# Optimization experiments

Measured on AMD Instinct MI355X. Metric: run time of the kernel, lower is better.

Reference implementation:

```python
import jax, jax.numpy as jnp
import numpy as np

SEMA_DIM = 1024
L1, L2, B = 256, 320, 64


def setup_inputs() -> dict:
    key = jax.random.key(0)
    k1, k2, kw1, kb1, kw2, kb2 = jax.random.split(key, 6)
    D = SEMA_DIM
    s = 1.0 / np.sqrt(D)
    return {
        "r1": jax.random.normal(k1, (L1, B, D), dtype=jnp.float32),
        "r2": jax.random.normal(k2, (L2, B, D), dtype=jnp.float32),
        "W1": jax.random.uniform(kw1, (D, D), jnp.float32, -s, s),
        "b1": jax.random.uniform(kb1, (D,), jnp.float32, -s, s),
        "W2": jax.random.uniform(kw2, (D, D), jnp.float32, -s, s),
        "b2": jax.random.uniform(kb2, (D,), jnp.float32, -s, s),
    }


def _mlp(x, W1, b1, W2, b2):
    # torch Linear: x @ W.T + b
    h = jax.nn.relu(x @ W1.T + b1)
    return h @ W2.T + b2


def reference(r1, r2, W1, b1, W2, b2):
    # (L, B, D) -> mlp -> (B, L, D)
    r1 = jnp.transpose(_mlp(r1, W1, b1, W2, b2), (1, 0, 2))  # [B, L1, D]
    r2 = jnp.transpose(_mlp(r2, W1, b1, W2, b2), (1, 0, 2))  # [B, L2, D]

    o = jnp.einsum("bid,bjd->bij", r1, r2)  # [B, L1, L2]
    o1 = jax.nn.softmax(o, axis=2)           # attend r1 -> r2
    o2 = jax.nn.softmax(o, axis=1)           # attend r2 -> r1

    r1_c = jnp.einsum("bij,bjd->bid", o1, r2)  # [B, L1, D]
    r2_c = jnp.einsum("bij,bid->bjd", o2, r1)  # [B, L2, D]

    r1_pool = jnp.concatenate([r1, r1_c], axis=-1).sum(axis=1) / r1.shape[1]  # [B, 2D]
    r2_pool = jnp.concatenate([r2, r2_c], axis=-1).sum(axis=1) / r2.shape[1]  # [B, 2D]
    return (r1_pool, r2_pool)
```

## Files before the change

kernel.cpp:

```cpp
#include <hip/hip_runtime.h>
#include <stdint.h>

#define L1C 256
#define L2C 320
#define BC  64
#define DC  1024

typedef __bf16 bf16_t;
typedef __bf16 bf16x8 __attribute__((ext_vector_type(8)));
typedef __bf16 bf16x4 __attribute__((ext_vector_type(4)));
typedef float  f32x4  __attribute__((ext_vector_type(4)));

__device__ __forceinline__ void gload16(const void* g, void* l) {
  __builtin_amdgcn_global_load_lds(
      (__attribute__((address_space(1))) void*)g,
      (__attribute__((address_space(3))) void*)l, 16, 0, 0);
}

__global__ __launch_bounds__(256)
void conv_kernel(const float* __restrict__ src, bf16_t* __restrict__ dst, int n4) {
  int i = blockIdx.x * 256 + threadIdx.x;
  const int stride = gridDim.x * 256;
  for (; i < n4; i += stride) {
    float4 v = ((const float4*)src)[i];
    bf16x4 o = { (__bf16)v.x, (__bf16)v.y, (__bf16)v.z, (__bf16)v.w };
    ((bf16x4*)dst)[i] = o;
  }
}

__global__ __launch_bounds__(512, 2)
void mlp_gemm8(const bf16_t* __restrict__ A, const bf16_t* __restrict__ W,
               const float* __restrict__ bias, bf16_t* __restrict__ C,
               int Mtiles, int relu) {
  const int nwg = Mtiles * 4;
  const int cpx = nwg >> 3;
  const int wg  = ((int)blockIdx.x & 7) * cpx + ((int)blockIdx.x >> 3);
  const int mt = wg >> 2, nt = wg & 3;

  __shared__ __align__(16) char lds[131072];

  const int t    = threadIdx.x;
  const int lane = t & 63, wid = t >> 6;
  const int wm = wid >> 2, wn = wid & 3;
  const int rsel = lane & 15, hi = lane >> 4;
  const int t16 = t * 16;

  const int P0 = t16, P1 = 8192 + t16;
  const int Lg0 = P0 ^ ((P0 >> 3) & 0x30);
  const int Lg1 = P1 ^ ((P1 >> 3) & 0x30);
  const int rS0 = Lg0 >> 6, cS0 = (Lg0 & 63) >> 1;
  const int rS1 = Lg1 >> 6, cS1 = (Lg1 & 63) >> 1;
  const bf16_t* pA0 = A + (size_t)(mt * 256 + rS0) * 1024 + cS0;
  const bf16_t* pA1 = A + (size_t)(mt * 256 + rS1) * 1024 + cS1;
  const bf16_t* pB0 = W + (size_t)(nt * 256 + rS0) * 1024 + cS0;
  const bf16_t* pB1 = W + (size_t)(nt * 256 + rS1) * 1024 + cS1;

  const int kchunk = (hi ^ ((rsel >> 1) & 3)) << 4;
  const int offA = ((wm * 128 + rsel) << 6) + kchunk;
  const int offB = 16384 + ((wn * 64 + rsel) << 6) + kchunk;

  f32x4 acc[8][4] = {};
  bf16x8 bfr[4];

#pragma unroll
  for (int p = 0; p < 3; ++p) {
    char* db = lds + p * 32768;
    gload16(pA0 + p * 32, db + t16);
    gload16(pA1 + p * 32, db + 8192 + t16);
    gload16(pB0 + p * 32, db + 16384 + t16);
    gload16(pB1 + p * 32, db + 24576 + t16);
  }
  asm volatile("s_waitcnt vmcnt(8)" ::: "memory");
  __builtin_amdgcn_s_barrier();
  __builtin_amdgcn_sched_barrier(0);

#pragma unroll 1
  for (int tt = 0; tt < 32; ++tt) {
    const char* rb = lds + (tt & 3) * 32768;
    char* sb = lds + ((tt + 3) & 3) * 32768;
    const int ks = (tt + 3) * 32;
    bf16x8 af[4];
#pragma unroll
    for (int m = 0; m < 4; ++m) af[m] = *(const bf16x8*)(rb + offA + m * 1024);
#pragma unroll
    for (int n = 0; n < 4; ++n) bfr[n] = *(const bf16x8*)(rb + offB + n * 1024);
    if (tt < 29) {
      gload16(pA0 + ks, sb + t16);
      gload16(pA1 + ks, sb + 8192 + t16);
    }
    __builtin_amdgcn_s_setprio(1);
#pragma unroll
    for (int m = 0; m < 4; ++m)
#pragma unroll
      for (int n = 0; n < 4; ++n)
        acc[m][n] = __builtin_amdgcn_mfma_f32_16x16x32_bf16(af[m], bfr[n], acc[m][n], 0, 0, 0);
    __builtin_amdgcn_s_setprio(0);
    __builtin_amdgcn_s_barrier();
    __builtin_amdgcn_sched_barrier(0);
#pragma unroll
    for (int m = 0; m < 4; ++m) af[m] = *(const bf16x8*)(rb + offA + (m + 4) * 1024);
    if (tt < 29) {
      gload16(pB0 + ks, sb + 16384 + t16);
      gload16(pB1 + ks, sb + 24576 + t16);
    }
    __builtin_amdgcn_s_setprio(1);
#pragma unroll
    for (int m = 0; m < 4; ++m)
#pragma unroll
      for (int n = 0; n < 4; ++n)
        acc[m + 4][n] = __builtin_amdgcn_mfma_f32_16x16x32_bf16(af[m], bfr[n], acc[m + 4][n], 0, 0, 0);
    __builtin_amdgcn_s_setprio(0);
    if (tt < 29)       asm volatile("s_waitcnt vmcnt(8)" ::: "memory");
    else if (tt == 29) asm volatile("s_waitcnt vmcnt(4)" ::: "memory");
    else if (tt == 30) asm volatile("s_waitcnt vmcnt(0)" ::: "memory");
    __builtin_amdgcn_s_barrier();
    __builtin_amdgcn_sched_barrier(0);
  }

  const int row0 = mt * 256 + wm * 128 + hi * 4;
  const int col0 = nt * 256 + wn * 64 + rsel;
  float bv[4];
#pragma unroll
  for (int n = 0; n < 4; ++n) bv[n] = bias[col0 + n * 16];
#pragma unroll
  for (int m = 0; m < 8; ++m) {
#pragma unroll
    for (int q = 0; q < 4; ++q) {
      const size_t rr = (size_t)(row0 + m * 16 + q) * 1024;
#pragma unroll
      for (int n = 0; n < 4; ++n) {
        float v = acc[m][n][q] + bv[n];
        if (relu) v = fmaxf(v, 0.f);
        C[rr + col0 + n * 16] = (bf16_t)v;
      }
    }
  }
}

__global__ __launch_bounds__(256)
void logits_gemm(const bf16_t* __restrict__ Y, float* __restrict__ O) {
  const int wg = ((int)blockIdx.x & 7) * 48 + ((int)blockIdx.x >> 3);
  const int b = wg / 6, t = wg % 6;
  const int mt = t / 3, nt = t % 3;

  const int f = threadIdx.x;
  const int lane = f & 63, w = f >> 6;
  const int sRow = f >> 2, sCol8 = (f & 3) * 8;

  const bf16_t* Y1 = Y;
  const bf16_t* Y2 = Y + (size_t)L1C * BC * DC;

  const int i0 = mt * 128 + sRow;
  const int i1 = i0 + 64;
  int j0 = nt * 128 + sRow;      if (j0 > L2C - 1) j0 = L2C - 1;
  int j1 = nt * 128 + sRow + 64; if (j1 > L2C - 1) j1 = L2C - 1;
  const bf16_t* A0 = Y1 + ((size_t)i0 * BC + b) * DC + sCol8;
  const bf16_t* A1 = Y1 + ((size_t)i1 * BC + b) * DC + sCol8;
  const bf16_t* B0 = Y2 + ((size_t)j0 * BC + b) * DC + sCol8;
  const bf16_t* B1 = Y2 + ((size_t)j1 * BC + b) * DC + sCol8;

  __shared__ __align__(16) bf16_t sA[128 * 32];
  __shared__ __align__(16) bf16_t sB[128 * 32];
  bf16_t* sAp = sA + sRow * 32 + sCol8;
  bf16_t* sBp = sB + sRow * 32 + sCol8;

  const int wr = (w >> 1) * 64, wc = (w & 1) * 64;
  const int rsel = lane & 15, koff = (lane >> 4) * 8;
  const bf16_t* rA = sA + (wr + rsel) * 32 + koff;
  const bf16_t* rB = sB + (wc + rsel) * 32 + koff;

  f32x4 acc[4][4] = {};
  for (int kt = 0; kt < 1024; kt += 32) {
    __syncthreads();
    gload16(A0 + kt, sAp);
    gload16(A1 + kt, sAp + 64 * 32);
    gload16(B0 + kt, sBp);
    gload16(B1 + kt, sBp + 64 * 32);
    asm volatile("s_waitcnt vmcnt(0)" ::: "memory");
    __syncthreads();
    bf16x8 af[4], bfv[4];
#pragma unroll
    for (int m = 0; m < 4; ++m) af[m] = *(const bf16x8*)(rA + m * 16 * 32);
#pragma unroll
    for (int n = 0; n < 4; ++n) bfv[n] = *(const bf16x8*)(rB + n * 16 * 32);
#pragma unroll
    for (int m = 0; m < 4; ++m)
#pragma unroll
      for (int n = 0; n < 4; ++n)
        acc[m][n] = __builtin_amdgcn_mfma_f32_16x16x32_bf16(af[m], bfv[n], acc[m][n], 0, 0, 0);
  }

  float* Ob = O + (size_t)b * L1C * L2C;
  const int row0 = mt * 128 + wr + (lane >> 4) * 4;
  const int col0 = nt * 128 + wc + rsel;
#pragma unroll
  for (int n = 0; n < 4; ++n) {
    const int c = col0 + n * 16;
    if (c < L2C) {
#pragma unroll
      for (int m = 0; m < 4; ++m) {
        const int r = row0 + m * 16;
#pragma unroll
        for (int q = 0; q < 4; ++q)
          Ob[(size_t)(r + q) * L2C + c] = acc[m][n][q];
      }
    }
  }
}

__global__ __launch_bounds__(256)
void row_stats(const float* __restrict__ O, float* __restrict__ rowM,
               float* __restrict__ rowInv) {
  const int gw = blockIdx.x * 4 + (threadIdx.x >> 6);
  const int lane = threadIdx.x & 63;
  const float* row = O + (size_t)gw * L2C;
  float v[5];
  float m = -1e30f;
#pragma unroll
  for (int t = 0; t < 5; ++t) { v[t] = row[t * 64 + lane]; m = fmaxf(m, v[t]); }
#pragma unroll
  for (int off = 32; off; off >>= 1) m = fmaxf(m, __shfl_xor(m, off));
  float s = 0.f;
#pragma unroll
  for (int t = 0; t < 5; ++t) s += __expf(v[t] - m);
#pragma unroll
  for (int off = 32; off; off >>= 1) s += __shfl_xor(s, off);
  if (lane == 0) { rowM[gw] = m; rowInv[gw] = 1.f / s; }
}

__global__ __launch_bounds__(256)
void col_stats_c1(const float* __restrict__ O, const float* __restrict__ rowM,
                  const float* __restrict__ rowInv, float* __restrict__ colM,
                  float* __restrict__ colInv, float* __restrict__ c1) {
  const int b = blockIdx.x / 5, jb = blockIdx.x % 5;
  const int jl = threadIdx.x & 63, ig = threadIdx.x >> 6;
  const int j = jb * 64 + jl;
  const float* Ob = O + (size_t)b * L1C * L2C + j;
  const float* rM = rowM + b * L1C;
  const float* rI = rowInv + b * L1C;
  float m = -1e30f, s = 0.f, cp = 0.f;
  for (int i = ig; i < L1C; i += 4) {
    float v = Ob[(size_t)i * L2C];
    float mn = fmaxf(m, v);
    s = s * __expf(m - mn) + __expf(v - mn);
    m = mn;
    cp += __expf(v - rM[i]) * rI[i];
  }
  __shared__ float sm[4][64], ss[4][64], sc[4][64];
  sm[ig][jl] = m; ss[ig][jl] = s; sc[ig][jl] = cp;
  __syncthreads();
  if (ig == 0) {
    for (int g = 1; g < 4; ++g) {
      float mg = sm[g][jl], sg = ss[g][jl];
      float mn = fmaxf(m, mg);
      s = s * __expf(m - mn) + sg * __expf(mg - mn);
      m = mn;
      cp += sc[g][jl];
    }
    colM[b * L2C + j] = m;
    colInv[b * L2C + j] = 1.f / s;
    c1[b * L2C + j] = cp;
  }
}

__global__ __launch_bounds__(256)
void c2_kernel(const float* __restrict__ O, const float* __restrict__ colM,
               const float* __restrict__ colInv, float* __restrict__ c2) {
  const int gw = blockIdx.x * 4 + (threadIdx.x >> 6);
  const int lane = threadIdx.x & 63;
  const int b = gw >> 8;
  const float* row = O + (size_t)gw * L2C;
  const float* cM = colM + b * L2C;
  const float* cI = colInv + b * L2C;
  float s = 0.f;
#pragma unroll
  for (int t = 0; t < 5; ++t) {
    const int j = t * 64 + lane;
    s += __expf(row[j] - cM[j]) * cI[j];
  }
#pragma unroll
  for (int off = 32; off; off >>= 1) s += __shfl_xor(s, off);
  if (lane == 0) c2[gw] = s;
}

__global__ __launch_bounds__(256)
void pool_y1(const bf16_t* __restrict__ Y1, const float* __restrict__ c2,
             float* __restrict__ out) {
  const int b = blockIdx.x >> 2;
  const int d = (blockIdx.x & 3) * 256 + threadIdx.x;
  float s1 = 0.f, s2 = 0.f;
  const float* c2b = c2 + b * L1C;
  for (int i = 0; i < L1C; ++i) {
    float v = (float)Y1[((size_t)i * BC + b) * DC + d];
    s1 += v;
    s2 += c2b[i] * v;
  }
  out[(size_t)b * 2048 + d] = s1 * (1.f / L1C);
  out[(size_t)BC * 2048 + (size_t)b * 2048 + 1024 + d] = s2 * (1.f / L2C);
}

__global__ __launch_bounds__(256)
void pool_y2(const bf16_t* __restrict__ Y2, const float* __restrict__ c1,
             float* __restrict__ out) {
  const int b = blockIdx.x >> 2;
  const int d = (blockIdx.x & 3) * 256 + threadIdx.x;
  float s1 = 0.f, s2 = 0.f;
  const float* c1b = c1 + b * L2C;
  for (int j = 0; j < L2C; ++j) {
    float v = (float)Y2[((size_t)j * BC + b) * DC + d];
    s1 += v;
    s2 += c1b[j] * v;
  }
  out[(size_t)BC * 2048 + (size_t)b * 2048 + d] = s1 * (1.f / L2C);
  out[(size_t)b * 2048 + 1024 + d] = s2 * (1.f / L1C);
}

extern "C" void kernel_launch(void* const* d_in, const int* in_sizes, int n_in,
                              void* d_out, int out_size, void* d_ws, size_t ws_size,
                              hipStream_t stream) {
  const float* r1 = (const float*)d_in[0];
  const float* r2 = (const float*)d_in[1];
  const float* W1 = (const float*)d_in[2];
  const float* b1 = (const float*)d_in[3];
  const float* W2 = (const float*)d_in[4];
  const float* b2 = (const float*)d_in[5];
  float* out = (float*)d_out;
  char* ws = (char*)d_ws;

  const size_t M1 = (size_t)L1C * BC;
  const size_t M2 = (size_t)L2C * BC;
  const size_t Mt = M1 + M2;

  size_t off = 0;
  bf16_t* XB  = (bf16_t*)(ws + off); off += Mt * DC * 2;
  bf16_t* HB  = (bf16_t*)(ws + off); off += Mt * DC * 2;
  bf16_t* WB1 = (bf16_t*)(ws + off); off += (size_t)DC * DC * 2;
  bf16_t* WB2 = (bf16_t*)(ws + off); off += (size_t)DC * DC * 2;
  float* rowM   = (float*)(ws + off); off += 65536;
  float* rowInv = (float*)(ws + off); off += 65536;
  float* colM   = (float*)(ws + off); off += 81920;
  float* colInv = (float*)(ws + off); off += 81920;
  float* c1v    = (float*)(ws + off); off += 81920;
  float* c2v    = (float*)(ws + off); off += 65536;

  bf16_t* YB = XB;
  float*  O  = (float*)HB;

  conv_kernel<<<2048, 256, 0, stream>>>(r1, XB,            (int)(M1 * DC / 4));
  conv_kernel<<<2048, 256, 0, stream>>>(r2, XB + M1 * DC,  (int)(M2 * DC / 4));
  conv_kernel<<<512,  256, 0, stream>>>(W1, WB1, (int)((size_t)DC * DC / 4));
  conv_kernel<<<512,  256, 0, stream>>>(W2, WB2, (int)((size_t)DC * DC / 4));

  mlp_gemm8<<<576, 512, 0, stream>>>(XB, WB1, b1, HB, 144, 1);
  mlp_gemm8<<<576, 512, 0, stream>>>(HB, WB2, b2, YB, 144, 0);

  logits_gemm<<<384, 256, 0, stream>>>(YB, O);

  row_stats<<<4096, 256, 0, stream>>>(O, rowM, rowInv);
  col_stats_c1<<<320, 256, 0, stream>>>(O, rowM, rowInv, colM, colInv, c1v);
  c2_kernel<<<4096, 256, 0, stream>>>(O, colM, colInv, c2v);

  pool_y1<<<256, 256, 0, stream>>>(YB, c2v, out);
  pool_y2<<<256, 256, 0, stream>>>(YB + M1 * DC, c1v, out);
}
```

Before: 331.2 us.

## Refactor logits and pooling algebraically through W2 to skip second MLP GEMM

Expresses the logits as H1·(W2ᵀW2)·H2ᵀ plus per-row and per-column bias terms (H·W2ᵀb2), so the full second MLP layer over all L1+L2 rows is no longer computed. The pooled outputs are built by pooling H first and applying W2 to only 256 pooled rows in a small GEMM. The cost is extra precomputation: a W2 transpose, a Gram-matrix GEMM, a bias-projection vector, and bias terms threaded through the softmax stats kernels. It also adds bf16 rounding of the Gram matrix and of the pooled vectors, and the pool GEMM runs on only 16 workgroups.

```diff
diff --git a/kernel.cpp b/kernel.cpp
--- a/kernel.cpp
+++ b/kernel.cpp
@@ -25,6 +25,39 @@
     float4 v = ((const float4*)src)[i];
     bf16x4 o = { (__bf16)v.x, (__bf16)v.y, (__bf16)v.z, (__bf16)v.w };
     ((bf16x4*)dst)[i] = o;
+  }
+}
+
+__global__ __launch_bounds__(256)
+void w2t_kernel(const float* __restrict__ W2, bf16_t* __restrict__ W2T) {
+  __shared__ float tile[32][33];
+  const int tx = threadIdx.x & 31, ty = threadIdx.x >> 5;
+  const int x0 = blockIdx.x * 32, y0 = blockIdx.y * 32;
+#pragma unroll
+  for (int k = 0; k < 32; k += 8)
+    tile[ty + k][tx] = W2[(size_t)(y0 + ty + k) * 1024 + x0 + tx];
+  __syncthreads();
+#pragma unroll
+  for (int k = 0; k < 32; k += 8)
+    W2T[(size_t)(x0 + ty + k) * 1024 + y0 + tx] = (bf16_t)tile[tx][ty + k];
+}
+
+__global__ __launch_bounds__(256)
+void wb_kernel(const float* __restrict__ W2, const float* __restrict__ b2,
+               float* __restrict__ w2b) {
+  const int dt = threadIdx.x & 15, kg = threadIdx.x >> 4;
+  const int d = blockIdx.x * 16 + dt;
+  float s = 0.f;
+  for (int k = kg * 64; k < kg * 64 + 64; ++k)
+    s += W2[(size_t)k * 1024 + d] * b2[k];
+  __shared__ float red[16][17];
+  red[kg][dt] = s;
+  __syncthreads();
+  if (kg == 0) {
+    float t = 0.f;
+#pragma unroll
+    for (int g = 0; g < 16; ++g) t += red[g][dt];
+    w2b[d] = t;
   }
 }
 
@@ -138,7 +171,160 @@
 }
 
 __global__ __launch_bounds__(256)
-void logits_gemm(const bf16_t* __restrict__ Y, float* __restrict__ O) {
+void mlp_gemm(const bf16_t* __restrict__ A, const bf16_t* __restrict__ W,
+              const float* __restrict__ bias, bf16_t* __restrict__ C,
+              int Mtiles, int relu) {
+  const int nwg = Mtiles * 8;
+  const int wg  = ((int)blockIdx.x & 7) * (nwg >> 3) + ((int)blockIdx.x >> 3);
+  const int mt = wg >> 3, nt = wg & 7;
+
+  const int f = threadIdx.x;
+  const int lane = f & 63, w = f >> 6;
+  const int sRow = f >> 2, sCol8 = (f & 3) * 8;
+
+  const bf16_t* Ab = A + (size_t)mt * 128 * 1024 + (size_t)sRow * 1024 + sCol8;
+  const bf16_t* Bb = W + (size_t)nt * 128 * 1024 + (size_t)sRow * 1024 + sCol8;
+
+  __shared__ __align__(16) bf16_t sA[128 * 32];
+  __shared__ __align__(16) bf16_t sB[128 * 32];
+  bf16_t* sAp = sA + sRow * 32 + sCol8;
+  bf16_t* sBp = sB + sRow * 32 + sCol8;
+
+  const int wr = (w >> 1) * 64, wc = (w & 1) * 64;
+  const int rsel = lane & 15, koff = (lane >> 4) * 8;
+  const bf16_t* rA = sA + (wr + rsel) * 32 + koff;
+  const bf16_t* rB = sB + (wc + rsel) * 32 + koff;
+
+  f32x4 acc[4][4] = {};
+  for (int kt = 0; kt < 1024; kt += 32) {
+    __syncthreads();
+    gload16(Ab + kt,             sAp);
+    gload16(Ab + kt + 64 * 1024, sAp + 64 * 32);
+    gload16(Bb + kt,             sBp);
+    gload16(Bb + kt + 64 * 1024, sBp + 64 * 32);
+    asm volatile("s_waitcnt vmcnt(0)" ::: "memory");
+    __syncthreads();
+    bf16x8 af[4], bfv[4];
+#pragma unroll
+    for (int m = 0; m < 4; ++m) af[m] = *(const bf16x8*)(rA + m * 16 * 32);
+#pragma unroll
+    for (int n = 0; n < 4; ++n) bfv[n] = *(const bf16x8*)(rB + n * 16 * 32);
+#pragma unroll
+    for (int m = 0; m < 4; ++m)
+#pragma unroll
+      for (int n = 0; n < 4; ++n)
+        acc[m][n] = __builtin_amdgcn_mfma_f32_16x16x32_bf16(af[m], bfv[n], acc[m][n], 0, 0, 0);
+  }
+
+  const int row0 = mt * 128 + wr + (lane >> 4) * 4;
+  const int col0 = nt * 128 + wc + rsel;
+#pragma unroll
+  for (int n = 0; n < 4; ++n) {
+    const int c = col0 + n * 16;
+    const float bv = bias[c];
+#pragma unroll
+    for (int m = 0; m < 4; ++m) {
+      const int r = row0 + m * 16;
+#pragma unroll
+      for (int q = 0; q < 4; ++q) {
+        float v = acc[m][n][q] + bv;
+        if (relu) v = fmaxf(v, 0.f);
+        C[(size_t)(r + q) * 1024 + c] = (bf16_t)v;
+      }
+    }
+  }
+}
+
+__global__ __launch_bounds__(256)
+void pool_gemm(const bf16_t* __restrict__ A, const bf16_t* __restrict__ W,
+               const float* __restrict__ bias, float* __restrict__ out) {
+  const int nwg = 16;
+  const int wg  = ((int)blockIdx.x & 7) * (nwg >> 3) + ((int)blockIdx.x >> 3);
+  const int mt = wg >> 3, nt = wg & 7;
+
+  const int f = threadIdx.x;
+  const int lane = f & 63, w = f >> 6;
+  const int sRow = f >> 2, sCol8 = (f & 3) * 8;
+
+  const bf16_t* Ab = A + (size_t)mt * 128 * 1024 + (size_t)sRow * 1024 + sCol8;
+  const bf16_t* Bb = W + (size_t)nt * 128 * 1024 + (size_t)sRow * 1024 + sCol8;
+
+  __shared__ __align__(16) bf16_t sA[128 * 32];
+  __shared__ __align__(16) bf16_t sB[128 * 32];
+  bf16_t* sAp = sA + sRow * 32 + sCol8;
+  bf16_t* sBp = sB + sRow * 32 + sCol8;
+
+  const int wr = (w >> 1) * 64, wc = (w & 1) * 64;
+  const int rsel = lane & 15, koff = (lane >> 4) * 8;
+  const bf16_t* rA = sA + (wr + rsel) * 32 + koff;
+  const bf16_t* rB = sB + (wc + rsel) * 32 + koff;
+
+  f32x4 acc[4][4] = {};
+  for (int kt = 0; kt < 1024; kt += 32) {
+    __syncthreads();
+    gload16(Ab + kt,             sAp);
+    gload16(Ab + kt + 64 * 1024, sAp + 64 * 32);
+    gload16(Bb + kt,             sBp);
+    gload16(Bb + kt + 64 * 1024, sBp + 64 * 32);
+    asm volatile("s_waitcnt vmcnt(0)" ::: "memory");
+    __syncthreads();
+    bf16x8 af[4], bfv[4];
+#pragma unroll
+    for (int m = 0; m < 4; ++m) af[m] = *(const bf16x8*)(rA + m * 16 * 32);
+#pragma unroll
+    for (int n = 0; n < 4; ++n) bfv[n] = *(const bf16x8*)(rB + n * 16 * 32);
+#pragma unroll
+    for (int m = 0; m < 4; ++m)
+#pragma unroll
+      for (int n = 0; n < 4; ++n)
+        acc[m][n] = __builtin_amdgcn_mfma_f32_16x16x32_bf16(af[m], bfv[n], acc[m][n], 0, 0, 0);
+  }
+
+  const int row0 = mt * 128 + wr + (lane >> 4) * 4;
+  const int col0 = nt * 128 + wc + rsel;
+#pragma unroll
+  for (int n = 0; n < 4; ++n) {
+    const int c = col0 + n * 16;
+    const float bv = bias[c];
+#pragma unroll
+    for (int m = 0; m < 4; ++m) {
+      const int r = row0 + m * 16;
+#pragma unroll
+      for (int q = 0; q < 4; ++q) {
+        const int rg = r + q;
+        const size_t oo = (size_t)(rg >> 7) * 131072 + (size_t)(rg & 63) * 2048 +
+                          ((rg >> 6) & 1) * 1024 + c;
+        out[oo] = acc[m][n][q] + bv;
+      }
+    }
+  }
+}
+
+__global__ __launch_bounds__(256)
+void t_kernel(const bf16_t* __restrict__ H, const float* __restrict__ w2b,
+              float* __restrict__ tT1, float* __restrict__ tT2) {
+  const int wv = threadIdx.x >> 6, lane = threadIdx.x & 63;
+  const int r = blockIdx.x * 4 + wv;
+  const bf16_t* hrow = H + (size_t)r * 1024;
+  float s = 0.f;
+#pragma unroll
+  for (int h = 0; h < 2; ++h) {
+    bf16x8 v = *(const bf16x8*)(hrow + h * 512 + lane * 8);
+#pragma unroll
+    for (int e = 0; e < 8; ++e) s += (float)v[e] * w2b[h * 512 + lane * 8 + e];
+  }
+#pragma unroll
+  for (int off = 32; off; off >>= 1) s += __shfl_xor(s, off);
+  if (lane == 0) {
+    const int b = r & 63;
+    if (r < 16384) tT1[b * L1C + (r >> 6)] = s;
+    else           tT2[b * L2C + ((r - 16384) >> 6)] = s;
+  }
+}
+
+__global__ __launch_bounds__(256)
+void logits_gemm(const bf16_t* __restrict__ Y1, const bf16_t* __restrict__ Y2,
+                 float* __restrict__ O) {
   const int wg = ((int)blockIdx.x & 7) * 48 + ((int)blockIdx.x >> 3);
   const int b = wg / 6, t = wg % 6;
   const int mt = t / 3, nt = t % 3;
@@ -146,9 +332,6 @@
   const int f = threadIdx.x;
   const int lane = f & 63, w = f >> 6;
   const int sRow = f >> 2, sCol8 = (f & 3) * 8;
-
-  const bf16_t* Y1 = Y;
-  const bf16_t* Y2 = Y + (size_t)L1C * BC * DC;
 
   const int i0 = mt * 128 + sRow;
   const int i1 = i0 + 64;
@@ -209,15 +392,17 @@
 }
 
 __global__ __launch_bounds__(256)
-void row_stats(const float* __restrict__ O, float* __restrict__ rowM,
-               float* __restrict__ rowInv) {
+void row_stats(const float* __restrict__ O, const float* __restrict__ tT2,
+               float* __restrict__ rowM, float* __restrict__ rowInv) {
   const int gw = blockIdx.x * 4 + (threadIdx.x >> 6);
   const int lane = threadIdx.x & 63;
+  const int b = gw >> 8;
   const float* row = O + (size_t)gw * L2C;
+  const float* t2 = tT2 + b * L2C;
   float v[5];
   float m = -1e30f;
 #pragma unroll
-  for (int t = 0; t < 5; ++t) { v[t] = row[t * 64 + lane]; m = fmaxf(m, v[t]); }
+  for (int t = 0; t < 5; ++t) { v[t] = row[t * 64 + lane] + t2[t * 64 + lane]; m = fmaxf(m, v[t]); }
 #pragma unroll
   for (int off = 32; off; off >>= 1) m = fmaxf(m, __shfl_xor(m, off));
   float s = 0.f;
@@ -229,22 +414,27 @@
 }
 
 __global__ __launch_bounds__(256)
-void col_stats_c1(const float* __restrict__ O, const float* __restrict__ rowM,
-                  const float* __restrict__ rowInv, float* __restrict__ colM,
-                  float* __restrict__ colInv, float* __restrict__ c1) {
+void col_stats_c1(const float* __restrict__ O, const float* __restrict__ tT1,
+                  const float* __restrict__ tT2,
+                  const float* __restrict__ rowM, const float* __restrict__ rowInv,
+                  float* __restrict__ colM, float* __restrict__ colInv,
+                  float* __restrict__ c1) {
   const int b = blockIdx.x / 5, jb = blockIdx.x % 5;
   const int jl = threadIdx.x & 63, ig = threadIdx.x >> 6;
   const int j = jb * 64 + jl;
   const float* Ob = O + (size_t)b * L1C * L2C + j;
   const float* rM = rowM + b * L1C;
   const float* rI = rowInv + b * L1C;
+  const float* t1 = tT1 + b * L1C;
+  const float t2j = tT2[b * L2C + j];
   float m = -1e30f, s = 0.f, cp = 0.f;
   for (int i = ig; i < L1C; i += 4) {
-    float v = Ob[(size_t)i * L2C];
+    float ov = Ob[(size_t)i * L2C];
+    float v = ov + t1[i];
     float mn = fmaxf(m, v);
     s = s * __expf(m - mn) + __expf(v - mn);
     m = mn;
-    cp += __expf(v - rM[i]) * rI[i];
+    cp += __expf(ov + t2j - rM[i]) * rI[i];
   }
   __shared__ float sm[4][64], ss[4][64], sc[4][64];
   sm[ig][jl] = m; ss[ig][jl] = s; sc[ig][jl] = cp;
@@ -264,19 +454,21 @@
 }
 
 __global__ __launch_bounds__(256)
-void c2_kernel(const float* __restrict__ O, const float* __restrict__ colM,
-               const float* __restrict__ colInv, float* __restrict__ c2) {
+void c2_kernel(const float* __restrict__ O, const float* __restrict__ tT1,
+               const float* __restrict__ colM, const float* __restrict__ colInv,
+               float* __restrict__ c2) {
   const int gw = blockIdx.x * 4 + (threadIdx.x >> 6);
   const int lane = threadIdx.x & 63;
   const int b = gw >> 8;
   const float* row = O + (size_t)gw * L2C;
   const float* cM = colM + b * L2C;
   const float* cI = colInv + b * L2C;
+  const float t1i = tT1[b * L1C + (gw & 255)];
   float s = 0.f;
 #pragma unroll
   for (int t = 0; t < 5; ++t) {
     const int j = t * 64 + lane;
-    s += __expf(row[j] - cM[j]) * cI[j];
+    s += __expf(row[j] + t1i - cM[j]) * cI[j];
   }
 #pragma unroll
   for (int off = 32; off; off >>= 1) s += __shfl_xor(s, off);
@@ -284,35 +476,26 @@
 }
 
 __global__ __launch_bounds__(256)
-void pool_y1(const bf16_t* __restrict__ Y1, const float* __restrict__ c2,
-             float* __restrict__ out) {
+void u_kernel(const bf16_t* __restrict__ H, const float* __restrict__ c1,
+              const float* __restrict__ c2, bf16_t* __restrict__ Ub) {
   const int b = blockIdx.x >> 2;
   const int d = (blockIdx.x & 3) * 256 + threadIdx.x;
-  float s1 = 0.f, s2 = 0.f;
+  const bf16_t* H2 = H + (size_t)L1C * BC * DC;
+  float s1 = 0.f, s1c = 0.f, s2 = 0.f, s2c = 0.f;
   const float* c2b = c2 + b * L1C;
   for (int i = 0; i < L1C; ++i) {
-    float v = (float)Y1[((size_t)i * BC + b) * DC + d];
-    s1 += v;
-    s2 += c2b[i] * v;
-  }
-  out[(size_t)b * 2048 + d] = s1 * (1.f / L1C);
-  out[(size_t)BC * 2048 + (size_t)b * 2048 + 1024 + d] = s2 * (1.f / L2C);
-}
-
-__global__ __launch_bounds__(256)
-void pool_y2(const bf16_t* __restrict__ Y2, const float* __restrict__ c1,
-             float* __restrict__ out) {
-  const int b = blockIdx.x >> 2;
-  const int d = (blockIdx.x & 3) * 256 + threadIdx.x;
-  float s1 = 0.f, s2 = 0.f;
+    float v = (float)H[((size_t)i * BC + b) * DC + d];
+    s1 += v; s1c += c2b[i] * v;
+  }
   const float* c1b = c1 + b * L2C;
   for (int j = 0; j < L2C; ++j) {
-    float v = (float)Y2[((size_t)j * BC + b) * DC + d];
-    s1 += v;
-    s2 += c1b[j] * v;
-  }
-  out[(size_t)BC * 2048 + (size_t)b * 2048 + d] = s1 * (1.f / L2C);
-  out[(size_t)b * 2048 + 1024 + d] = s2 * (1.f / L1C);
+    float v = (float)H2[((size_t)j * BC + b) * DC + d];
+    s2 += v; s2c += c1b[j] * v;
+  }
+  Ub[(size_t)(0 * 64 + b) * 1024 + d] = (bf16_t)(s1  * (1.f / L1C));
+  Ub[(size_t)(1 * 64 + b) * 1024 + d] = (bf16_t)(s2c * (1.f / L1C));
+  Ub[(size_t)(2 * 64 + b) * 1024 + d] = (bf16_t)(s2  * (1.f / L2C));
+  Ub[(size_t)(3 * 64 + b) * 1024 + d] = (bf16_t)(s1c * (1.f / L2C));
 }
 
 extern "C" void kernel_launch(void* const* d_in, const int* in_sizes, int n_in,
@@ -336,30 +519,45 @@
   bf16_t* HB  = (bf16_t*)(ws + off); off += Mt * DC * 2;
   bf16_t* WB1 = (bf16_t*)(ws + off); off += (size_t)DC * DC * 2;
   bf16_t* WB2 = (bf16_t*)(ws + off); off += (size_t)DC * DC * 2;
-  float* rowM   = (float*)(ws + off); off += 65536;
-  float* rowInv = (float*)(ws + off); off += 65536;
-  float* colM   = (float*)(ws + off); off += 81920;
-  float* colInv = (float*)(ws + off); off += 81920;
-  float* c1v    = (float*)(ws + off); off += 81920;
-  float* c2v    = (float*)(ws + off); off += 65536;
-
-  bf16_t* YB = XB;
-  float*  O  = (float*)HB;
-
-  conv_kernel<<<2048, 256, 0, stream>>>(r1, XB,            (int)(M1 * DC / 4));
-  conv_kernel<<<2048, 256, 0, stream>>>(r2, XB + M1 * DC,  (int)(M2 * DC / 4));
+  bf16_t* W2T = (bf16_t*)(ws + off); off += (size_t)DC * DC * 2;
+  bf16_t* GB  = (bf16_t*)(ws + off); off += (size_t)DC * DC * 2;
+  float* w2b   = (float*)(ws + off); off += 4096;
+  float* zb    = (float*)(ws + off); off += 4096;
+  float* tT1   = (float*)(ws + off); off += BC * L1C * 4;
+  float* tT2   = (float*)(ws + off); off += BC * L2C * 4;
+  float* rowM  = (float*)(ws + off); off += BC * L1C * 4;
+  float* rowIv = (float*)(ws + off); off += BC * L1C * 4;
+  float* colM  = (float*)(ws + off); off += BC * L2C * 4;
+  float* colIv = (float*)(ws + off); off += BC * L2C * 4;
+  float* c1v   = (float*)(ws + off); off += BC * L2C * 4;
+  float* c2v   = (float*)(ws + off); off += BC * L1C * 4;
+  bf16_t* Ub   = (bf16_t*)(ws + off); off += 256 * DC * 2;
+
+  bf16_t* Z = XB;
+  float*  O = (float*)((char*)XB + 35651584);
+  bf16_t* H2 = HB + M1 * DC;
+
+  conv_kernel<<<2048, 256, 0, stream>>>(r1, XB,           (int)(M1 * DC / 4));
+  conv_kernel<<<2048, 256, 0, stream>>>(r2, XB + M1 * DC, (int)(M2 * DC / 4));
   conv_kernel<<<512,  256, 0, stream>>>(W1, WB1, (int)((size_t)DC * DC / 4));
   conv_kernel<<<512,  256, 0, stream>>>(W2, WB2, (int)((size_t)DC * DC / 4));
+  w2t_kernel<<<dim3(32, 32), 256, 0, stream>>>(W2, W2T);
+  wb_kernel<<<64, 256, 0, stream>>>(W2, b2, w2b);
+  hipMemsetAsync(zb, 0, 4096, stream);
 
   mlp_gemm8<<<576, 512, 0, stream>>>(XB, WB1, b1, HB, 144, 1);
-  mlp_gemm8<<<576, 512, 0, stream>>>(HB, WB2, b2, YB, 144, 0);
-
-  logits_gemm<<<384, 256, 0, stream>>>(YB, O);
-
-  row_stats<<<4096, 256, 0, stream>>>(O, rowM, rowInv);
-  col_stats_c1<<<320, 256, 0, stream>>>(O, rowM, rowInv, colM, colInv, c1v);
-  c2_kernel<<<4096, 256, 0, stream>>>(O, colM, colInv, c2v);
-
-  pool_y1<<<256, 256, 0, stream>>>(YB, c2v, out);
-  pool_y2<<<256, 256, 0, stream>>>(YB + M1 * DC, c1v, out);
-}
+
+  mlp_gemm<<<64, 256, 0, stream>>>(W2T, W2T, zb, GB, 8, 0);
+  t_kernel<<<9216, 256, 0, stream>>>(HB, w2b, tT1, tT2);
+
+  mlp_gemm8<<<256, 512, 0, stream>>>(HB, GB, zb, Z, 64, 0);
+
+  logits_gemm<<<384, 256, 0, stream>>>(Z, H2, O);
+
+  row_stats<<<4096, 256, 0, stream>>>(O, tT2, rowM, rowIv);
+  col_stats_c1<<<320, 256, 0, stream>>>(O, tT1, tT2, rowM, rowIv, colM, colIv, c1v);
+  c2_kernel<<<4096, 256, 0, stream>>>(O, tT1, colM, colIv, c2v);
+
+  u_kernel<<<256, 256, 0, stream>>>(HB, c1v, c2v, Ub);
+  pool_gemm<<<16, 256, 0, stream>>>(Ub, WB2, b2, out);
+}
```

Result: no change. 330.7 us (-0.2%).
